# Optimization experiments

Measured on AMD Instinct MI355X. Metric: run time of the kernel, lower is better.

## Reference

```python
import jax, jax.numpy as jnp
import numpy as np

EPS = 1e-8


def setup_inputs() -> dict:
    key = jax.random.key(0)
    k1, k2 = jax.random.split(key)
    N, D, K = 200000, 256, 64
    embeds = jax.random.normal(k1, (N, D), dtype=jnp.float32)
    init = jax.random.uniform(k2, (K, D), dtype=jnp.float32)  # torch.rand(K, n_h)
    beta = jnp.ones((1,), dtype=jnp.float32)
    return {"embeds": embeds, "init": init, "beta": beta, "num_iter": 11}


def reference(embeds, init, beta, num_iter):
    # embeds: [N, D], init: [K, D], beta: scalar temperature
    data_abs = jnp.linalg.norm(embeds, axis=1, keepdims=True)            # [N, 1]
    data_norm = embeds / jnp.maximum(data_abs, EPS)                      # [N, D]
    b = beta.reshape(())
    mu = init
    r = None
    for _ in range(num_iter):  # small fixed iteration count (default 11)
        mu_abs = jnp.linalg.norm(mu, axis=1, keepdims=True)              # [K, 1]
        mu_norm = mu / jnp.maximum(mu_abs, EPS)                          # [K, D]
        dist = data_norm @ mu_norm.T                                     # [N, K]
        r = jax.nn.softmax(b * dist, axis=1)                             # [N, K]
        cluster_r = r.sum(axis=0)                                        # [K]
        cluster_mean = r.T @ embeds                                      # [K, D]
        mu = cluster_mean / cluster_r[:, None]                           # diag(1/cluster_r) @ cluster_mean
    return mu, r
```

## Files before the change

kernel.cpp:

```cpp
#include <hip/hip_runtime.h>
#include <math.h>


#define N_ROWS 200000
#define DIM 256
#define KC 64
#define NUM_ITER 11
#define TR 64
#define NTILES (N_ROWS / TR)
#define EPSV 1e-8f
#define NB 256

typedef _Float16 half8 __attribute__((ext_vector_type(8)));
typedef _Float16 half4 __attribute__((ext_vector_type(4)));
typedef float f32x4 __attribute__((ext_vector_type(4)));

typedef __attribute__((address_space(3))) void as3_void;
typedef __attribute__((address_space(1))) void as1_void;

__device__ __forceinline__ void glds16(const void* g, void* l) {
  __builtin_amdgcn_global_load_lds((const as1_void*)g, (as3_void*)l, 16, 0, 0);
}

__device__ __forceinline__ float wave_reduce_sum(float v) {
#pragma unroll
  for (int off = 32; off > 0; off >>= 1) v += __shfl_xor(v, off, 64);
  return v;
}

__device__ __forceinline__ void barrier_lgkm_only() {
  __builtin_amdgcn_sched_barrier(0);
  asm volatile("s_waitcnt lgkmcnt(0)" ::: "memory");
  __builtin_amdgcn_s_barrier();
  __builtin_amdgcn_sched_barrier(0);
}

__global__ void rn_convert_kernel(const float* __restrict__ embeds,
                                  float* __restrict__ inv_norm,
                                  _Float16* __restrict__ Xh,
                                  const float* __restrict__ init,
                                  float* __restrict__ mu_raw,
                                  float* __restrict__ mu_ssq) {
  if (blockIdx.x == 0) {
    const int c = threadIdx.x >> 2, qq = threadIdx.x & 3;
    const float4* src = (const float4*)(init + (size_t)c * DIM + 64 * qq);
    float4* dst = (float4*)(mu_raw + (size_t)c * DIM + 64 * qq);
    float ss = 0.f;
#pragma unroll
    for (int i = 0; i < 16; ++i) {
      float4 v = src[i];
      dst[i] = v;
      ss = fmaf(v.x, v.x, ss); ss = fmaf(v.y, v.y, ss);
      ss = fmaf(v.z, v.z, ss); ss = fmaf(v.w, v.w, ss);
    }
    mu_ssq[c * 4 + qq] = ss;
  }
  int gw = (blockIdx.x * blockDim.x + threadIdx.x) >> 6;
  int lane = threadIdx.x & 63;
  int nw = (gridDim.x * blockDim.x) >> 6;
  for (int row = gw; row < N_ROWS; row += nw) {
    float4 v = *(const float4*)(embeds + (size_t)row * DIM + 4 * lane);
    float s = v.x * v.x;
    s = fmaf(v.y, v.y, s); s = fmaf(v.z, v.z, s); s = fmaf(v.w, v.w, s);
    s = wave_reduce_sum(s);
    if (lane == 0) inv_norm[row] = 1.0f / fmaxf(sqrtf(s), EPSV);
    half4 h;
    h[0] = (_Float16)v.x; h[1] = (_Float16)v.y; h[2] = (_Float16)v.z; h[3] = (_Float16)v.w;
    *(half4*)(Xh + (size_t)row * DIM + 4 * lane) = h;
  }
}

__device__ __forceinline__ void stage_row512_8(const _Float16* g, _Float16* l,
                                               int wid, int lane) {
#pragma unroll
  for (int ii = 0; ii < 4; ++ii) {
    int i = wid * 4 + ii;
    int row = i * 2 + (lane >> 5);
    int slot = (lane & 31) ^ (row & 7);
    glds16((const char*)g + row * 512 + slot * 16, (char*)l + i * 1024);
  }
}

template <int LAST>
__global__ __launch_bounds__(512, 2) void cluster_main8(
    const _Float16* __restrict__ Xh, const float* __restrict__ inv_norm,
    const float* __restrict__ beta, const float* __restrict__ mu_raw,
    const float* __restrict__ mu_ssq, float* __restrict__ part_cm,
    float* __restrict__ part_crt, float* __restrict__ r_out) {
  __shared__ alignas(16) _Float16 mu_lds[KC * DIM];
  __shared__ alignas(16) _Float16 x_lds[2][TR * DIM];
  __shared__ alignas(16) _Float16 xt_lds[DIM * TR];
  __shared__ alignas(16) _Float16 r_lds[KC * TR];
  __shared__ alignas(16) f32x4 dist_lds[16 * 64];
  __shared__ float cr_lds[4 * KC];

  const int tid = threadIdx.x, wid = tid >> 6, lane = tid & 63;
  const int l15 = lane & 15, h = lane >> 4;
  const int kh = wid >> 2, rg = wid & 3;
  const float b = beta[0];
  const int myrow = 16 * rg + l15;
  const int rb0 = blockIdx.x;

  stage_row512_8(Xh + (size_t)rb0 * TR * DIM, x_lds[0], wid, lane);

  if (tid < KC) {
    const float4 s4 = *(const float4*)&mu_ssq[4 * tid];
    cr_lds[tid] = 1.0f / fmaxf(sqrtf(s4.x + s4.y + s4.z + s4.w), EPSV);
  }
  __syncthreads();
  {
    const float4* mu_raw4 = (const float4*)mu_raw;
#pragma unroll
    for (int i = 0; i < 8; ++i) {
      const int idx = tid + 512 * i;
      const int cl = idx >> 6;
      const int dim0 = (idx & 63) * 4;
      float4 v = mu_raw4[idx];
      const float iv = cr_lds[cl];
      const int sw = dim0 ^ ((cl & 7) << 3);
      half4 hh;
      hh[0] = (_Float16)(v.x * iv); hh[1] = (_Float16)(v.y * iv);
      hh[2] = (_Float16)(v.z * iv); hh[3] = (_Float16)(v.w * iv);
      *(half4*)&mu_lds[cl * DIM + sw] = hh;
    }
  }
  __syncthreads();

  half8 amreg[4][4];
#pragma unroll
  for (int t = 0; t < 4; ++t) {
    const int kb = 128 * kh + 32 * t + 8 * h;
#pragma unroll
    for (int m = 0; m < 4; ++m) {
      const int cl = 16 * m + l15;
      amreg[t][m] = *(const half8*)&mu_lds[cl * DIM + (kb ^ ((cl & 7) << 3))];
    }
  }

  f32x4 acc2[4][2] = {};
  float cr_acc[16] = {};
  int p = 0;
  for (int rb = rb0; rb < NTILES; rb += NB, p ^= 1) {
    const int row0 = rb * TR;
    const int rbn = rb + NB;
    if (rbn < NTILES)
      stage_row512_8(Xh + (size_t)rbn * TR * DIM, x_lds[p ^ 1], wid, lane);

    f32x4 acc1[4] = {};
    const _Float16* xb = x_lds[p];
#pragma unroll
    for (int t = 0; t < 4; ++t) {
      const int kb = 128 * kh + 32 * t + 8 * h;
      half8 bx = *(const half8*)&xb[myrow * DIM + (kb ^ ((myrow & 7) << 3))];
#pragma unroll
      for (int m = 0; m < 4; ++m)
        acc1[m] = __builtin_amdgcn_mfma_f32_16x16x32_f16(amreg[t][m], bx, acc1[m], 0, 0, 0);
    }
    if (kh) {
#pragma unroll
      for (int m = 0; m < 4; ++m) dist_lds[(rg * 4 + m) * 64 + lane] = acc1[m];
    }
    barrier_lgkm_only();

    if (!kh) {
#pragma unroll
      for (int m = 0; m < 4; ++m) acc1[m] += dist_lds[(rg * 4 + m) * 64 + lane];
      const int xr = row0 + myrow;
      const float sc = b * inv_norm[xr];
#pragma unroll
      for (int m = 0; m < 4; ++m)
#pragma unroll
        for (int j = 0; j < 4; ++j) acc1[m][j] *= sc;
      float mx = -1e30f;
#pragma unroll
      for (int m = 0; m < 4; ++m)
#pragma unroll
        for (int j = 0; j < 4; ++j) mx = fmaxf(mx, acc1[m][j]);
      mx = fmaxf(mx, __shfl_xor(mx, 16));
      mx = fmaxf(mx, __shfl_xor(mx, 32));
      float esum = 0.f;
#pragma unroll
      for (int m = 0; m < 4; ++m)
#pragma unroll
        for (int j = 0; j < 4; ++j) {
          float e = __expf(acc1[m][j] - mx);
          acc1[m][j] = e;
          esum += e;
        }
      esum += __shfl_xor(esum, 16);
      esum += __shfl_xor(esum, 32);
      const float rcp = 1.0f / esum;
#pragma unroll
      for (int m = 0; m < 4; ++m) {
#pragma unroll
        for (int j = 0; j < 4; ++j) {
          const float rv = acc1[m][j] * rcp;
          acc1[m][j] = rv;
          const int cl = 16 * m + 4 * h + j;
          cr_acc[m * 4 + j] += rv;
          r_lds[cl * TR + (myrow ^ ((cl & 7) << 3))] = (_Float16)rv;
        }
        if (LAST)
          *(float4*)&r_out[(size_t)xr * KC + 16 * m + 4 * h] = *(float4*)&acc1[m];
      }
    } else {
      const int t8 = tid & 255;
      const int db = t8 >> 3, rb8 = t8 & 7;
      union U { uint4 v; unsigned u[4]; };
      U tin[8];
#pragma unroll
      for (int k2 = 0; k2 < 8; ++k2)
        tin[k2].v = *(const uint4*)&xb[(8 * rb8 + k2) * DIM + ((8 * db) ^ (k2 << 3))];
#pragma unroll
      for (int j = 0; j < 8; ++j) {
        const unsigned sel = (j & 1) ? 0x07060302u : 0x05040100u;
        U o;
#pragma unroll
        for (int m2 = 0; m2 < 4; ++m2)
          o.u[m2] = __builtin_amdgcn_perm(tin[2 * m2 + 1].u[j >> 1],
                                          tin[2 * m2].u[j >> 1], sel);
        *(uint4*)&xt_lds[(8 * db + j) * TR + 8 * (rb8 ^ j)] = o.v;
      }
    }

    barrier_lgkm_only();

#pragma unroll
    for (int t = 0; t < 2; ++t) {
      const int kb = 32 * t + 8 * h;
      half8 ar[4], bx2[2];
#pragma unroll
      for (int m = 0; m < 4; ++m) {
        const int cl = 16 * m + l15;
        ar[m] = *(const half8*)&r_lds[cl * TR + (kb ^ ((cl & 7) << 3))];
      }
#pragma unroll
      for (int n = 0; n < 2; ++n) {
        const int dm = 32 * wid + 16 * n + l15;
        bx2[n] = *(const half8*)&xt_lds[dm * TR + (kb ^ ((dm & 7) << 3))];
      }
#pragma unroll
      for (int m = 0; m < 4; ++m)
#pragma unroll
        for (int n = 0; n < 2; ++n)
          acc2[m][n] = __builtin_amdgcn_mfma_f32_16x16x32_f16(ar[m], bx2[n], acc2[m][n], 0, 0, 0);
    }
    __syncthreads();
  }

  float* pc = part_cm + (size_t)blockIdx.x * (KC * DIM);
#pragma unroll
  for (int m = 0; m < 4; ++m)
#pragma unroll
    for (int n = 0; n < 2; ++n)
#pragma unroll
      for (int j = 0; j < 4; ++j)
        pc[(16 * m + 4 * h + j) * DIM + 32 * wid + 16 * n + l15] = acc2[m][n][j];
  if (wid < 4) {
#pragma unroll
    for (int m = 0; m < 4; ++m)
#pragma unroll
      for (int j = 0; j < 4; ++j) {
        float v = cr_acc[m * 4 + j];
        v += __shfl_xor(v, 1); v += __shfl_xor(v, 2);
        v += __shfl_xor(v, 4); v += __shfl_xor(v, 8);
        if (l15 == 0) cr_lds[wid * KC + 16 * m + 4 * h + j] = v;
      }
  }
  __syncthreads();
  if (wid == 0)
    part_crt[(size_t)lane * NB + blockIdx.x] =
        cr_lds[lane] + cr_lds[KC + lane] + cr_lds[2 * KC + lane] + cr_lds[3 * KC + lane];
}

template <int FINAL>
__global__ void reduce_mu(const float* __restrict__ part_cm,
                          const float* __restrict__ part_crt,
                          float* __restrict__ mu_raw, float* __restrict__ mu_ssq,
                          float* __restrict__ mu_out) {
  const int cl = blockIdx.x, q = blockIdx.y;
  const int tid = threadIdx.x, wid = tid >> 6, lane = tid & 63;
  __shared__ float red2[4 * 64];
  __shared__ float cr4[4];
  float c = part_crt[(size_t)cl * NB + tid];
  c = wave_reduce_sum(c);
  if (lane == 0) cr4[wid] = c;
  float s = 0.f;
  const float* basep =
      part_cm + (size_t)(64 * wid) * (KC * DIM) + cl * DIM + 64 * q + lane;
#pragma unroll 8
  for (int i = 0; i < 64; ++i) s += basep[(size_t)i * (KC * DIM)];
  red2[wid * 64 + lane] = s;
  __syncthreads();
  if (wid == 0) {
    const float crv = cr4[0] + cr4[1] + cr4[2] + cr4[3];
    const float st = red2[lane] + red2[64 + lane] + red2[128 + lane] + red2[192 + lane];
    const float mu = st / crv;
    const int dim = 64 * q + lane;
    if (FINAL) {
      mu_out[cl * DIM + dim] = mu;
    } else {
      mu_raw[cl * DIM + dim] = mu;
      float ss = wave_reduce_sum(mu * mu);
      if (lane == 0) mu_ssq[cl * 4 + q] = ss;
    }
  }
}

__global__ void rownorm_v1(const float* __restrict__ embeds, float* __restrict__ inv_norm) {
  int gw = (blockIdx.x * blockDim.x + threadIdx.x) >> 6;
  int lane = threadIdx.x & 63;
  int nw = (gridDim.x * blockDim.x) >> 6;
  for (int row = gw; row < N_ROWS; row += nw) {
    const float* rp = embeds + (size_t)row * DIM;
    float s = 0.f;
#pragma unroll
    for (int j = 0; j < 4; ++j) { float v = rp[lane + 64 * j]; s = fmaf(v, v, s); }
    s = wave_reduce_sum(s);
    if (lane == 0) inv_norm[row] = 1.0f / fmaxf(sqrtf(s), EPSV);
  }
}
__global__ void prep0_v1(const float* __restrict__ init, float* __restrict__ muT) {
  int k = blockIdx.x, lane = threadIdx.x;
  const float* rp = init + k * DIM;
  float v[4]; float s = 0.f;
#pragma unroll
  for (int j = 0; j < 4; ++j) { v[j] = rp[lane + 64 * j]; s = fmaf(v[j], v[j], s); }
  s = wave_reduce_sum(s);
  float inv = 1.0f / fmaxf(sqrtf(s), EPSV);
#pragma unroll
  for (int j = 0; j < 4; ++j) muT[(lane + 64 * j) * KC + k] = v[j] * inv;
}
__device__ __forceinline__ float wave_reduce_max_v1(float v) {
#pragma unroll
  for (int off = 32; off > 0; off >>= 1) v = fmaxf(v, __shfl_xor(v, off, 64));
  return v;
}
template <int LAST>
__global__ __launch_bounds__(256, 1) void main_v1(
    const float* __restrict__ embeds, const float* __restrict__ inv_norm,
    const float* __restrict__ muT, const float* __restrict__ beta,
    float* __restrict__ part_cm, float* __restrict__ part_cr,
    float* __restrict__ r_out, int nb) {
  __shared__ float mu_l[DIM * KC];
  __shared__ float x_l[TR * DIM];
  __shared__ float r_l[TR * KC];
  __shared__ float cr_l[4 * KC];
  const int tid = threadIdx.x, wid = tid >> 6, lane = tid & 63;
  const float b = beta[0];
  {
    const float4* m4 = (const float4*)muT; float4* ml4 = (float4*)mu_l;
#pragma unroll
    for (int i = 0; i < 16; ++i) ml4[tid + i * 256] = m4[tid + i * 256];
  }
  float acc[64];
#pragma unroll
  for (int i = 0; i < 64; ++i) acc[i] = 0.f;
  float cr = 0.f;
  for (int rb = blockIdx.x; rb < NTILES; rb += nb) {
    const int row0 = rb * TR;
    __syncthreads();
    {
      const float4* x4 = (const float4*)(embeds + (size_t)row0 * DIM);
      float4* xl4 = (float4*)x_l;
#pragma unroll
      for (int i = 0; i < 16; ++i) xl4[tid + i * 256] = x4[tid + i * 256];
    }
    __syncthreads();
    float dist[16];
#pragma unroll
    for (int r = 0; r < 16; ++r) dist[r] = 0.f;
    const int rbase = wid * 16;
    for (int d = 0; d < DIM; d += 4) {
      float mv0 = mu_l[(d + 0) * KC + lane], mv1 = mu_l[(d + 1) * KC + lane];
      float mv2 = mu_l[(d + 2) * KC + lane], mv3 = mu_l[(d + 3) * KC + lane];
#pragma unroll
      for (int r = 0; r < 16; ++r) {
        float4 xv = *(const float4*)&x_l[(rbase + r) * DIM + d];
        dist[r] = fmaf(xv.x, mv0, dist[r]); dist[r] = fmaf(xv.y, mv1, dist[r]);
        dist[r] = fmaf(xv.z, mv2, dist[r]); dist[r] = fmaf(xv.w, mv3, dist[r]);
      }
    }
#pragma unroll
    for (int r = 0; r < 16; ++r) {
      const int row = rbase + r;
      float s = b * (dist[r] * inv_norm[row0 + row]);
      float m = wave_reduce_max_v1(s);
      float e = __expf(s - m);
      float sum = wave_reduce_sum(e);
      float rv = e * (1.0f / sum);
      cr += rv;
      r_l[row * KC + lane] = rv;
      if (LAST) r_out[(size_t)(row0 + row) * KC + lane] = rv;
    }
    __syncthreads();
    const int dbase = wid * 64;
    for (int row = 0; row < TR; ++row) {
      float rv = r_l[row * KC + lane];
#pragma unroll
      for (int dd = 0; dd < 64; dd += 4) {
        float4 xv = *(const float4*)&x_l[row * DIM + dbase + dd];
        acc[dd + 0] = fmaf(rv, xv.x, acc[dd + 0]); acc[dd + 1] = fmaf(rv, xv.y, acc[dd + 1]);
        acc[dd + 2] = fmaf(rv, xv.z, acc[dd + 2]); acc[dd + 3] = fmaf(rv, xv.w, acc[dd + 3]);
      }
    }
  }
  {
    float* pp = part_cm + ((size_t)blockIdx.x * KC + lane) * DIM + wid * 64;
#pragma unroll
    for (int dd = 0; dd < 64; dd += 4)
      *(float4*)&pp[dd] = make_float4(acc[dd], acc[dd + 1], acc[dd + 2], acc[dd + 3]);
    cr_l[wid * KC + lane] = cr;
  }
  __syncthreads();
  if (wid == 0) {
    float c = cr_l[lane] + cr_l[64 + lane] + cr_l[128 + lane] + cr_l[192 + lane];
    part_cr[(size_t)blockIdx.x * KC + lane] = c;
  }
}
template <int FINAL>
__global__ void reduce_v1(const float* __restrict__ part_cm, const float* __restrict__ part_cr,
                          float* __restrict__ muT, float* __restrict__ mu_out, int nb) {
  const int k = blockIdx.x, t = threadIdx.x;
  __shared__ float red[256];
  float s = 0.f;
  for (int bl = 0; bl < nb; ++bl) s += part_cm[((size_t)bl * KC + k) * DIM + t];
  float c = 0.f;
  for (int bl = t; bl < nb; bl += 256) c += part_cr[(size_t)bl * KC + k];
  red[t] = c; __syncthreads();
#pragma unroll
  for (int off = 128; off > 0; off >>= 1) { if (t < off) red[t] += red[t + off]; __syncthreads(); }
  const float crv = red[0]; __syncthreads();
  const float mu = s / crv;
  if (FINAL) { mu_out[k * DIM + t] = mu; return; }
  red[t] = mu * mu; __syncthreads();
#pragma unroll
  for (int off = 128; off > 0; off >>= 1) { if (t < off) red[t] += red[t + off]; __syncthreads(); }
  const float inv = 1.0f / fmaxf(sqrtf(red[0]), EPSV);
  muT[t * KC + k] = mu * inv;
}

extern "C" void kernel_launch(void* const* d_in, const int* in_sizes, int n_in,
                              void* d_out, int out_size, void* d_ws, size_t ws_size,
                              hipStream_t stream) {
  const float* embeds = (const float*)d_in[0];
  const float* init = (const float*)d_in[1];
  const float* beta = (const float*)d_in[2];
  float* out_mu = (float*)d_out;
  float* out_r = out_mu + KC * DIM;
  char* ws = (char*)d_ws;

  const size_t szX = (size_t)N_ROWS * DIM * 2;
  const size_t szInv = (size_t)N_ROWS * 4;
  const size_t szMuR = (size_t)KC * DIM * 4;
  const size_t szSsq = (size_t)KC * 4 * 4;
  const size_t szPC = (size_t)NB * KC * DIM * 4;
  const size_t szPR = (size_t)KC * NB * 4;
  const size_t need = szX + szInv + szMuR + szSsq + szPC + szPR;

  if (ws_size >= need) {
    char* pp = ws;
    _Float16* Xh = (_Float16*)pp; pp += szX;
    float* invn = (float*)pp; pp += szInv;
    float* mu_raw = (float*)pp; pp += szMuR;
    float* mu_ssq = (float*)pp; pp += szSsq;
    float* pcm = (float*)pp; pp += szPC;
    float* pcrt = (float*)pp;

    rn_convert_kernel<<<2048, 256, 0, stream>>>(embeds, invn, Xh, init, mu_raw, mu_ssq);
    for (int it = 0; it < NUM_ITER; ++it) {
      if (it > 0)
        reduce_mu<0><<<dim3(KC, 4), 256, 0, stream>>>(pcm, pcrt, mu_raw, mu_ssq, nullptr);
      if (it == NUM_ITER - 1)
        cluster_main8<1><<<NB, 512, 0, stream>>>(Xh, invn, beta, mu_raw, mu_ssq,
                                                 pcm, pcrt, out_r);
      else
        cluster_main8<0><<<NB, 512, 0, stream>>>(Xh, invn, beta, mu_raw, mu_ssq,
                                                 pcm, pcrt, out_r);
    }
    reduce_mu<1><<<dim3(KC, 4), 256, 0, stream>>>(pcm, pcrt, nullptr, nullptr, out_mu);
  } else {
    float* wsf = (float*)d_ws;
    float* muT = wsf;
    float* invn = muT + DIM * KC;
    size_t avail = ws_size / sizeof(float);
    size_t fixed = (size_t)DIM * KC + N_ROWS;
    size_t per_blk = (size_t)KC * DIM + KC;
    int nb = 256;
    if (avail > fixed) {
      size_t mx = (avail - fixed) / per_blk;
      if (mx < 256) nb = (int)mx;
    } else nb = 1;
    if (nb < 1) nb = 1;
    float* pcm = invn + N_ROWS;
    float* pcr = pcm + (size_t)nb * KC * DIM;

    rownorm_v1<<<2048, 256, 0, stream>>>(embeds, invn);
    prep0_v1<<<KC, 64, 0, stream>>>(init, muT);
    for (int it = 0; it < NUM_ITER; ++it) {
      if (it > 0) reduce_v1<0><<<KC, 256, 0, stream>>>(pcm, pcr, muT, nullptr, nb);
      if (it == NUM_ITER - 1)
        main_v1<1><<<nb, 256, 0, stream>>>(embeds, invn, muT, beta, pcm, pcr, out_r, nb);
      else
        main_v1<0><<<nb, 256, 0, stream>>>(embeds, invn, muT, beta, pcm, pcr, nullptr, nb);
    }
    reduce_v1<1><<<KC, 256, 0, stream>>>(pcm, pcr, muT, out_mu, nb);
  }
}
```

Measured before the change: 498.4 us.

## Restructure cluster kernel to 256-thread blocks with full-K per wave, 512 blocks

```diff
diff --git a/kernel.cpp b/kernel.cpp
--- a/kernel.cpp
+++ b/kernel.cpp
@@ -9,7 +9,7 @@
 #define TR 64
 #define NTILES (N_ROWS / TR)
 #define EPSV 1e-8f
-#define NB 256
+#define NB2 512
 
 typedef _Float16 half8 __attribute__((ext_vector_type(8)));
 typedef _Float16 half4 __attribute__((ext_vector_type(4)));
@@ -70,11 +70,11 @@
   }
 }
 
-__device__ __forceinline__ void stage_row512_8(const _Float16* g, _Float16* l,
+__device__ __forceinline__ void stage_row512_4(const _Float16* g, _Float16* l,
                                                int wid, int lane) {
 #pragma unroll
-  for (int ii = 0; ii < 4; ++ii) {
-    int i = wid * 4 + ii;
+  for (int ii = 0; ii < 8; ++ii) {
+    int i = wid * 8 + ii;
     int row = i * 2 + (lane >> 5);
     int slot = (lane & 31) ^ (row & 7);
     glds16((const char*)g + row * 512 + slot * 16, (char*)l + i * 1024);
@@ -82,26 +82,23 @@
 }
 
 template <int LAST>
-__global__ __launch_bounds__(512, 2) void cluster_main8(
+__global__ __launch_bounds__(256, 2) void cluster_main2b(
     const _Float16* __restrict__ Xh, const float* __restrict__ inv_norm,
     const float* __restrict__ beta, const float* __restrict__ mu_raw,
     const float* __restrict__ mu_ssq, float* __restrict__ part_cm,
     float* __restrict__ part_crt, float* __restrict__ r_out) {
-  __shared__ alignas(16) _Float16 mu_lds[KC * DIM];
-  __shared__ alignas(16) _Float16 x_lds[2][TR * DIM];
+  __shared__ alignas(16) _Float16 x_lds[TR * DIM];
   __shared__ alignas(16) _Float16 xt_lds[DIM * TR];
   __shared__ alignas(16) _Float16 r_lds[KC * TR];
-  __shared__ alignas(16) f32x4 dist_lds[16 * 64];
   __shared__ float cr_lds[4 * KC];
 
   const int tid = threadIdx.x, wid = tid >> 6, lane = tid & 63;
   const int l15 = lane & 15, h = lane >> 4;
-  const int kh = wid >> 2, rg = wid & 3;
   const float b = beta[0];
-  const int myrow = 16 * rg + l15;
+  const int myrow = 16 * wid + l15;
   const int rb0 = blockIdx.x;
 
-  stage_row512_8(Xh + (size_t)rb0 * TR * DIM, x_lds[0], wid, lane);
+  stage_row512_4(Xh + (size_t)rb0 * TR * DIM, x_lds, wid, lane);
 
   if (tid < KC) {
     const float4 s4 = *(const float4*)&mu_ssq[4 * tid];
@@ -111,8 +108,8 @@
   {
     const float4* mu_raw4 = (const float4*)mu_raw;
 #pragma unroll
-    for (int i = 0; i < 8; ++i) {
-      const int idx = tid + 512 * i;
+    for (int i = 0; i < 16; ++i) {
+      const int idx = tid + 256 * i;
       const int cl = idx >> 6;
       const int dim0 = (idx & 63) * 4;
       float4 v = mu_raw4[idx];
@@ -121,52 +118,40 @@
       half4 hh;
       hh[0] = (_Float16)(v.x * iv); hh[1] = (_Float16)(v.y * iv);
       hh[2] = (_Float16)(v.z * iv); hh[3] = (_Float16)(v.w * iv);
-      *(half4*)&mu_lds[cl * DIM + sw] = hh;
+      *(half4*)&xt_lds[cl * DIM + sw] = hh;
     }
   }
   __syncthreads();
-
-  half8 amreg[4][4];
-#pragma unroll
-  for (int t = 0; t < 4; ++t) {
-    const int kb = 128 * kh + 32 * t + 8 * h;
+  half8 amreg[8][4];
+#pragma unroll
+  for (int t = 0; t < 8; ++t) {
+    const int kb = 32 * t + 8 * h;
 #pragma unroll
     for (int m = 0; m < 4; ++m) {
       const int cl = 16 * m + l15;
-      amreg[t][m] = *(const half8*)&mu_lds[cl * DIM + (kb ^ ((cl & 7) << 3))];
-    }
-  }
-
-  f32x4 acc2[4][2] = {};
+      amreg[t][m] = *(const half8*)&xt_lds[cl * DIM + (kb ^ ((cl & 7) << 3))];
+    }
+  }
+  barrier_lgkm_only();
+
+  f32x4 acc2[4][4] = {};
   float cr_acc[16] = {};
-  int p = 0;
-  for (int rb = rb0; rb < NTILES; rb += NB, p ^= 1) {
-    const int row0 = rb * TR;
-    const int rbn = rb + NB;
-    if (rbn < NTILES)
-      stage_row512_8(Xh + (size_t)rbn * TR * DIM, x_lds[p ^ 1], wid, lane);
+  for (int rb = rb0; rb < NTILES; rb += NB2) {
+    const int xr = rb * TR + myrow;
+    const float invn = inv_norm[xr];
 
     f32x4 acc1[4] = {};
-    const _Float16* xb = x_lds[p];
-#pragma unroll
-    for (int t = 0; t < 4; ++t) {
-      const int kb = 128 * kh + 32 * t + 8 * h;
-      half8 bx = *(const half8*)&xb[myrow * DIM + (kb ^ ((myrow & 7) << 3))];
+#pragma unroll
+    for (int t = 0; t < 8; ++t) {
+      const int kb = 32 * t + 8 * h;
+      half8 bx = *(const half8*)&x_lds[myrow * DIM + (kb ^ ((myrow & 7) << 3))];
 #pragma unroll
       for (int m = 0; m < 4; ++m)
         acc1[m] = __builtin_amdgcn_mfma_f32_16x16x32_f16(amreg[t][m], bx, acc1[m], 0, 0, 0);
     }
-    if (kh) {
-#pragma unroll
-      for (int m = 0; m < 4; ++m) dist_lds[(rg * 4 + m) * 64 + lane] = acc1[m];
-    }
-    barrier_lgkm_only();
-
-    if (!kh) {
-#pragma unroll
-      for (int m = 0; m < 4; ++m) acc1[m] += dist_lds[(rg * 4 + m) * 64 + lane];
-      const int xr = row0 + myrow;
-      const float sc = b * inv_norm[xr];
+
+    {
+      const float sc = b * invn;
 #pragma unroll
       for (int m = 0; m < 4; ++m)
 #pragma unroll
@@ -203,14 +188,15 @@
         if (LAST)
           *(float4*)&r_out[(size_t)xr * KC + 16 * m + 4 * h] = *(float4*)&acc1[m];
       }
-    } else {
-      const int t8 = tid & 255;
-      const int db = t8 >> 3, rb8 = t8 & 7;
+    }
+
+    {
+      const int db = tid >> 3, rb8 = tid & 7;
       union U { uint4 v; unsigned u[4]; };
       U tin[8];
 #pragma unroll
       for (int k2 = 0; k2 < 8; ++k2)
-        tin[k2].v = *(const uint4*)&xb[(8 * rb8 + k2) * DIM + ((8 * db) ^ (k2 << 3))];
+        tin[k2].v = *(const uint4*)&x_lds[(8 * rb8 + k2) * DIM + ((8 * db) ^ (k2 << 3))];
 #pragma unroll
       for (int j = 0; j < 8; ++j) {
         const unsigned sel = (j & 1) ? 0x07060302u : 0x05040100u;
@@ -225,24 +211,27 @@
 
     barrier_lgkm_only();
 
+    if (rb + NB2 < NTILES)
+      stage_row512_4(Xh + (size_t)(rb + NB2) * TR * DIM, x_lds, wid, lane);
+
 #pragma unroll
     for (int t = 0; t < 2; ++t) {
       const int kb = 32 * t + 8 * h;
-      half8 ar[4], bx2[2];
+      half8 ar[4], bx2[4];
 #pragma unroll
       for (int m = 0; m < 4; ++m) {
         const int cl = 16 * m + l15;
         ar[m] = *(const half8*)&r_lds[cl * TR + (kb ^ ((cl & 7) << 3))];
       }
 #pragma unroll
-      for (int n = 0; n < 2; ++n) {
-        const int dm = 32 * wid + 16 * n + l15;
+      for (int n = 0; n < 4; ++n) {
+        const int dm = 64 * wid + 16 * n + l15;
         bx2[n] = *(const half8*)&xt_lds[dm * TR + (kb ^ ((dm & 7) << 3))];
       }
 #pragma unroll
       for (int m = 0; m < 4; ++m)
 #pragma unroll
-        for (int n = 0; n < 2; ++n)
+        for (int n = 0; n < 4; ++n)
           acc2[m][n] = __builtin_amdgcn_mfma_f32_16x16x32_f16(ar[m], bx2[n], acc2[m][n], 0, 0, 0);
     }
     __syncthreads();
@@ -252,24 +241,22 @@
 #pragma unroll
   for (int m = 0; m < 4; ++m)
 #pragma unroll
-    for (int n = 0; n < 2; ++n)
+    for (int n = 0; n < 4; ++n)
 #pragma unroll
       for (int j = 0; j < 4; ++j)
-        pc[(16 * m + 4 * h + j) * DIM + 32 * wid + 16 * n + l15] = acc2[m][n][j];
-  if (wid < 4) {
-#pragma unroll
-    for (int m = 0; m < 4; ++m)
-#pragma unroll
-      for (int j = 0; j < 4; ++j) {
-        float v = cr_acc[m * 4 + j];
-        v += __shfl_xor(v, 1); v += __shfl_xor(v, 2);
-        v += __shfl_xor(v, 4); v += __shfl_xor(v, 8);
-        if (l15 == 0) cr_lds[wid * KC + 16 * m + 4 * h + j] = v;
-      }
-  }
+        pc[(16 * m + 4 * h + j) * DIM + 64 * wid + 16 * n + l15] = acc2[m][n][j];
+#pragma unroll
+  for (int m = 0; m < 4; ++m)
+#pragma unroll
+    for (int j = 0; j < 4; ++j) {
+      float v = cr_acc[m * 4 + j];
+      v += __shfl_xor(v, 1); v += __shfl_xor(v, 2);
+      v += __shfl_xor(v, 4); v += __shfl_xor(v, 8);
+      if (l15 == 0) cr_lds[wid * KC + 16 * m + 4 * h + j] = v;
+    }
   __syncthreads();
   if (wid == 0)
-    part_crt[(size_t)lane * NB + blockIdx.x] =
+    part_crt[(size_t)lane * NB2 + blockIdx.x] =
         cr_lds[lane] + cr_lds[KC + lane] + cr_lds[2 * KC + lane] + cr_lds[3 * KC + lane];
 }
 
@@ -282,14 +269,15 @@
   const int tid = threadIdx.x, wid = tid >> 6, lane = tid & 63;
   __shared__ float red2[4 * 64];
   __shared__ float cr4[4];
-  float c = part_crt[(size_t)cl * NB + tid];
+  float c = part_crt[(size_t)cl * NB2 + tid] +
+            part_crt[(size_t)cl * NB2 + 256 + tid];
   c = wave_reduce_sum(c);
   if (lane == 0) cr4[wid] = c;
   float s = 0.f;
   const float* basep =
-      part_cm + (size_t)(64 * wid) * (KC * DIM) + cl * DIM + 64 * q + lane;
+      part_cm + (size_t)(128 * wid) * (KC * DIM) + cl * DIM + 64 * q + lane;
 #pragma unroll 8
-  for (int i = 0; i < 64; ++i) s += basep[(size_t)i * (KC * DIM)];
+  for (int i = 0; i < 128; ++i) s += basep[(size_t)i * (KC * DIM)];
   red2[wid * 64 + lane] = s;
   __syncthreads();
   if (wid == 0) {
@@ -307,6 +295,7 @@
   }
 }
 
+#define NTILES64 NTILES
 __global__ void rownorm_v1(const float* __restrict__ embeds, float* __restrict__ inv_norm) {
   int gw = (blockIdx.x * blockDim.x + threadIdx.x) >> 6;
   int lane = threadIdx.x & 63;
@@ -357,7 +346,7 @@
 #pragma unroll
   for (int i = 0; i < 64; ++i) acc[i] = 0.f;
   float cr = 0.f;
-  for (int rb = blockIdx.x; rb < NTILES; rb += nb) {
+  for (int rb = blockIdx.x; rb < NTILES64; rb += nb) {
     const int row0 = rb * TR;
     __syncthreads();
     {
@@ -454,8 +443,8 @@
   const size_t szInv = (size_t)N_ROWS * 4;
   const size_t szMuR = (size_t)KC * DIM * 4;
   const size_t szSsq = (size_t)KC * 4 * 4;
-  const size_t szPC = (size_t)NB * KC * DIM * 4;
-  const size_t szPR = (size_t)KC * NB * 4;
+  const size_t szPC = (size_t)NB2 * KC * DIM * 4;
+  const size_t szPR = (size_t)KC * NB2 * 4;
   const size_t need = szX + szInv + szMuR + szSsq + szPC + szPR;
 
   if (ws_size >= need) {
@@ -472,11 +461,11 @@
       if (it > 0)
         reduce_mu<0><<<dim3(KC, 4), 256, 0, stream>>>(pcm, pcrt, mu_raw, mu_ssq, nullptr);
       if (it == NUM_ITER - 1)
-        cluster_main8<1><<<NB, 512, 0, stream>>>(Xh, invn, beta, mu_raw, mu_ssq,
-                                                 pcm, pcrt, out_r);
+        cluster_main2b<1><<<NB2, 256, 0, stream>>>(Xh, invn, beta, mu_raw, mu_ssq,
+                                                   pcm, pcrt, out_r);
       else
-        cluster_main8<0><<<NB, 512, 0, stream>>>(Xh, invn, beta, mu_raw, mu_ssq,
-                                                 pcm, pcrt, out_r);
+        cluster_main2b<0><<<NB2, 256, 0, stream>>>(Xh, invn, beta, mu_raw, mu_ssq,
+                                                   pcm, pcrt, out_r);
     }
     reduce_mu<1><<<dim3(KC, 4), 256, 0, stream>>>(pcm, pcrt, nullptr, nullptr, out_mu);
   } else {
```

Measured after the change: 1.038 ms. 2.08x slower.

## Fuse fp16 conversion and row-norm pass into the first clustering iteration

Applied to the files above, without the earlier changes.

```diff
diff --git a/kernel.cpp b/kernel.cpp
--- a/kernel.cpp
+++ b/kernel.cpp
@@ -35,41 +35,6 @@
   __builtin_amdgcn_sched_barrier(0);
 }
 
-__global__ void rn_convert_kernel(const float* __restrict__ embeds,
-                                  float* __restrict__ inv_norm,
-                                  _Float16* __restrict__ Xh,
-                                  const float* __restrict__ init,
-                                  float* __restrict__ mu_raw,
-                                  float* __restrict__ mu_ssq) {
-  if (blockIdx.x == 0) {
-    const int c = threadIdx.x >> 2, qq = threadIdx.x & 3;
-    const float4* src = (const float4*)(init + (size_t)c * DIM + 64 * qq);
-    float4* dst = (float4*)(mu_raw + (size_t)c * DIM + 64 * qq);
-    float ss = 0.f;
-#pragma unroll
-    for (int i = 0; i < 16; ++i) {
-      float4 v = src[i];
-      dst[i] = v;
-      ss = fmaf(v.x, v.x, ss); ss = fmaf(v.y, v.y, ss);
-      ss = fmaf(v.z, v.z, ss); ss = fmaf(v.w, v.w, ss);
-    }
-    mu_ssq[c * 4 + qq] = ss;
-  }
-  int gw = (blockIdx.x * blockDim.x + threadIdx.x) >> 6;
-  int lane = threadIdx.x & 63;
-  int nw = (gridDim.x * blockDim.x) >> 6;
-  for (int row = gw; row < N_ROWS; row += nw) {
-    float4 v = *(const float4*)(embeds + (size_t)row * DIM + 4 * lane);
-    float s = v.x * v.x;
-    s = fmaf(v.y, v.y, s); s = fmaf(v.z, v.z, s); s = fmaf(v.w, v.w, s);
-    s = wave_reduce_sum(s);
-    if (lane == 0) inv_norm[row] = 1.0f / fmaxf(sqrtf(s), EPSV);
-    half4 h;
-    h[0] = (_Float16)v.x; h[1] = (_Float16)v.y; h[2] = (_Float16)v.z; h[3] = (_Float16)v.w;
-    *(half4*)(Xh + (size_t)row * DIM + 4 * lane) = h;
-  }
-}
-
 __device__ __forceinline__ void stage_row512_8(const _Float16* g, _Float16* l,
                                                int wid, int lane) {
 #pragma unroll
@@ -79,6 +44,236 @@
     int slot = (lane & 31) ^ (row & 7);
     glds16((const char*)g + row * 512 + slot * 16, (char*)l + i * 1024);
   }
+}
+
+__global__ __launch_bounds__(512, 1) void cluster_first(
+    const float* __restrict__ embeds, const float* __restrict__ init,
+    const float* __restrict__ beta, _Float16* __restrict__ Xh,
+    float* __restrict__ inv_norm, float* __restrict__ part_cm,
+    float* __restrict__ part_crt) {
+  __shared__ alignas(16) _Float16 x_lds[2][TR * DIM];
+  __shared__ alignas(16) _Float16 xt_lds[DIM * TR];
+  __shared__ alignas(16) _Float16 mu_lds[KC * DIM];
+  __shared__ alignas(16) _Float16 r_lds[KC * TR];
+  __shared__ alignas(16) f32x4 dist_lds[16 * 64];
+  __shared__ float cr_lds[4 * KC];
+  __shared__ float inv_lds[TR];
+
+  float* x32 = (float*)&x_lds[0][0];
+  _Float16* xtile = xt_lds;
+  _Float16* xtr = &x_lds[0][0];
+
+  const int tid = threadIdx.x, wid = tid >> 6, lane = tid & 63;
+  const int l15 = lane & 15, h = lane >> 4;
+  const int kh = wid >> 2, rg = wid & 3;
+  const float b = beta[0];
+  const int myrow = 16 * rg + l15;
+  const int rb0 = blockIdx.x;
+
+  {
+    const int cl = tid >> 3, sub = tid & 7;
+    float ss = 0.f;
+#pragma unroll
+    for (int j = 0; j < 8; ++j) {
+      float4 v = *(const float4*)(init + (size_t)cl * DIM + sub * 32 + 4 * j);
+      ss = fmaf(v.x, v.x, ss); ss = fmaf(v.y, v.y, ss);
+      ss = fmaf(v.z, v.z, ss); ss = fmaf(v.w, v.w, ss);
+    }
+    ss += __shfl_xor(ss, 1); ss += __shfl_xor(ss, 2); ss += __shfl_xor(ss, 4);
+    if (sub == 0) cr_lds[cl] = ss;
+  }
+  __syncthreads();
+  if (tid < KC) cr_lds[tid] = 1.0f / fmaxf(sqrtf(cr_lds[tid]), EPSV);
+  __syncthreads();
+  {
+    const float4* init4 = (const float4*)init;
+#pragma unroll
+    for (int i = 0; i < 8; ++i) {
+      const int idx = tid + 512 * i;
+      const int cl = idx >> 6;
+      const int dim0 = (idx & 63) * 4;
+      float4 v = init4[idx];
+      const float iv = cr_lds[cl];
+      const int sw = dim0 ^ ((cl & 7) << 3);
+      half4 hh;
+      hh[0] = (_Float16)(v.x * iv); hh[1] = (_Float16)(v.y * iv);
+      hh[2] = (_Float16)(v.z * iv); hh[3] = (_Float16)(v.w * iv);
+      *(half4*)&mu_lds[cl * DIM + sw] = hh;
+    }
+  }
+  __syncthreads();
+  half8 amreg[4][4];
+#pragma unroll
+  for (int t = 0; t < 4; ++t) {
+    const int kb = 128 * kh + 32 * t + 8 * h;
+#pragma unroll
+    for (int m = 0; m < 4; ++m) {
+      const int cl = 16 * m + l15;
+      amreg[t][m] = *(const half8*)&mu_lds[cl * DIM + (kb ^ ((cl & 7) << 3))];
+    }
+  }
+
+  f32x4 acc2[4][2] = {};
+  float cr_acc[16] = {};
+  for (int rb = rb0; rb < NTILES; rb += NB) {
+#pragma unroll
+    for (int ii = 0; ii < 8; ++ii) {
+      const int row = wid * 8 + ii;
+      const int slot = lane ^ (row & 7);
+      glds16((const char*)embeds + (size_t)(rb * TR + row) * 1024 + slot * 16,
+             (char*)x32 + row * 1024);
+    }
+    __syncthreads();
+
+    {
+      const int row = tid >> 3, sub = tid & 7;
+      float ss = 0.f;
+      half8 hh[4];
+#pragma unroll
+      for (int i2 = 0; i2 < 8; ++i2) {
+        const int g = sub * 8 + i2;
+        float4 v = *(const float4*)((const char*)x32 + row * 1024 +
+                                    ((g ^ (row & 7)) * 16));
+        ss = fmaf(v.x, v.x, ss); ss = fmaf(v.y, v.y, ss);
+        ss = fmaf(v.z, v.z, ss); ss = fmaf(v.w, v.w, ss);
+        _Float16* hp = (_Float16*)&hh[i2 >> 1] + (i2 & 1) * 4;
+        hp[0] = (_Float16)v.x; hp[1] = (_Float16)v.y;
+        hp[2] = (_Float16)v.z; hp[3] = (_Float16)v.w;
+      }
+#pragma unroll
+      for (int j = 0; j < 4; ++j) {
+        const int slot = (sub * 4 + j) ^ (row & 7);
+        *(half8*)((char*)xtile + row * 512 + slot * 16) = hh[j];
+        *(float4*)((char*)Xh + (size_t)(rb * TR + row) * 512 + sub * 64 + j * 16) =
+            *(float4*)&hh[j];
+      }
+      ss += __shfl_xor(ss, 1); ss += __shfl_xor(ss, 2); ss += __shfl_xor(ss, 4);
+      if (sub == 0) {
+        const float iv = 1.0f / fmaxf(sqrtf(ss), EPSV);
+        inv_lds[row] = iv;
+        inv_norm[rb * TR + row] = iv;
+      }
+    }
+    barrier_lgkm_only();
+
+    f32x4 acc1[4] = {};
+#pragma unroll
+    for (int t = 0; t < 4; ++t) {
+      const int kb = 128 * kh + 32 * t + 8 * h;
+      half8 bx = *(const half8*)&xtile[myrow * DIM + (kb ^ ((myrow & 7) << 3))];
+#pragma unroll
+      for (int m = 0; m < 4; ++m)
+        acc1[m] = __builtin_amdgcn_mfma_f32_16x16x32_f16(amreg[t][m], bx, acc1[m], 0, 0, 0);
+    }
+    if (kh) {
+#pragma unroll
+      for (int m = 0; m < 4; ++m) dist_lds[(rg * 4 + m) * 64 + lane] = acc1[m];
+    }
+    barrier_lgkm_only();
+
+    if (!kh) {
+#pragma unroll
+      for (int m = 0; m < 4; ++m) acc1[m] += dist_lds[(rg * 4 + m) * 64 + lane];
+      const float sc = b * inv_lds[myrow];
+#pragma unroll
+      for (int m = 0; m < 4; ++m)
+#pragma unroll
+        for (int j = 0; j < 4; ++j) acc1[m][j] *= sc;
+      float mx = -1e30f;
+#pragma unroll
+      for (int m = 0; m < 4; ++m)
+#pragma unroll
+        for (int j = 0; j < 4; ++j) mx = fmaxf(mx, acc1[m][j]);
+      mx = fmaxf(mx, __shfl_xor(mx, 16));
+      mx = fmaxf(mx, __shfl_xor(mx, 32));
+      float esum = 0.f;
+#pragma unroll
+      for (int m = 0; m < 4; ++m)
+#pragma unroll
+        for (int j = 0; j < 4; ++j) {
+          float e = __expf(acc1[m][j] - mx);
+          acc1[m][j] = e;
+          esum += e;
+        }
+      esum += __shfl_xor(esum, 16);
+      esum += __shfl_xor(esum, 32);
+      const float rcp = 1.0f / esum;
+#pragma unroll
+      for (int m = 0; m < 4; ++m)
+#pragma unroll
+        for (int j = 0; j < 4; ++j) {
+          const float rv = acc1[m][j] * rcp;
+          const int cl = 16 * m + 4 * h + j;
+          cr_acc[m * 4 + j] += rv;
+          r_lds[cl * TR + (myrow ^ ((cl & 7) << 3))] = (_Float16)rv;
+        }
+    } else {
+      const int t8 = tid & 255;
+      const int db = t8 >> 3, rb8 = t8 & 7;
+      union U { uint4 v; unsigned u[4]; };
+      U tin[8];
+#pragma unroll
+      for (int k2 = 0; k2 < 8; ++k2)
+        tin[k2].v = *(const uint4*)&xtile[(8 * rb8 + k2) * DIM + ((8 * db) ^ (k2 << 3))];
+#pragma unroll
+      for (int j = 0; j < 8; ++j) {
+        const unsigned sel = (j & 1) ? 0x07060302u : 0x05040100u;
+        U o;
+#pragma unroll
+        for (int m2 = 0; m2 < 4; ++m2)
+          o.u[m2] = __builtin_amdgcn_perm(tin[2 * m2 + 1].u[j >> 1],
+                                          tin[2 * m2].u[j >> 1], sel);
+        *(uint4*)&xtr[(8 * db + j) * TR + 8 * (rb8 ^ j)] = o.v;
+      }
+    }
+    barrier_lgkm_only();
+
+#pragma unroll
+    for (int t = 0; t < 2; ++t) {
+      const int kb = 32 * t + 8 * h;
+      half8 ar[4], bx2[2];
+#pragma unroll
+      for (int m = 0; m < 4; ++m) {
+        const int cl = 16 * m + l15;
+        ar[m] = *(const half8*)&r_lds[cl * TR + (kb ^ ((cl & 7) << 3))];
+      }
+#pragma unroll
+      for (int n = 0; n < 2; ++n) {
+        const int dm = 32 * wid + 16 * n + l15;
+        bx2[n] = *(const half8*)&xtr[dm * TR + (kb ^ ((dm & 7) << 3))];
+      }
+#pragma unroll
+      for (int m = 0; m < 4; ++m)
+#pragma unroll
+        for (int n = 0; n < 2; ++n)
+          acc2[m][n] = __builtin_amdgcn_mfma_f32_16x16x32_f16(ar[m], bx2[n], acc2[m][n], 0, 0, 0);
+    }
+    __syncthreads();
+  }
+
+  float* pc = part_cm + (size_t)blockIdx.x * (KC * DIM);
+#pragma unroll
+  for (int m = 0; m < 4; ++m)
+#pragma unroll
+    for (int n = 0; n < 2; ++n)
+#pragma unroll
+      for (int j = 0; j < 4; ++j)
+        pc[(16 * m + 4 * h + j) * DIM + 32 * wid + 16 * n + l15] = acc2[m][n][j];
+  if (wid < 4) {
+#pragma unroll
+    for (int m = 0; m < 4; ++m)
+#pragma unroll
+      for (int j = 0; j < 4; ++j) {
+        float v = cr_acc[m * 4 + j];
+        v += __shfl_xor(v, 1); v += __shfl_xor(v, 2);
+        v += __shfl_xor(v, 4); v += __shfl_xor(v, 8);
+        if (l15 == 0) cr_lds[wid * KC + 16 * m + 4 * h + j] = v;
+      }
+  }
+  __syncthreads();
+  if (wid == 0)
+    part_crt[(size_t)lane * NB + blockIdx.x] =
+        cr_lds[lane] + cr_lds[KC + lane] + cr_lds[2 * KC + lane] + cr_lds[3 * KC + lane];
 }
 
 template <int LAST>
@@ -467,10 +662,9 @@
     float* pcm = (float*)pp; pp += szPC;
     float* pcrt = (float*)pp;
 
-    rn_convert_kernel<<<2048, 256, 0, stream>>>(embeds, invn, Xh, init, mu_raw, mu_ssq);
-    for (int it = 0; it < NUM_ITER; ++it) {
-      if (it > 0)
-        reduce_mu<0><<<dim3(KC, 4), 256, 0, stream>>>(pcm, pcrt, mu_raw, mu_ssq, nullptr);
+    cluster_first<<<NB, 512, 0, stream>>>(embeds, init, beta, Xh, invn, pcm, pcrt);
+    for (int it = 1; it < NUM_ITER; ++it) {
+      reduce_mu<0><<<dim3(KC, 4), 256, 0, stream>>>(pcm, pcrt, mu_raw, mu_ssq, nullptr);
       if (it == NUM_ITER - 1)
         cluster_main8<1><<<NB, 512, 0, stream>>>(Xh, invn, beta, mu_raw, mu_ssq,
                                                  pcm, pcrt, out_r);
```

Measured after the change: 490.7 us, median of 2. Within noise of the previous version (-1.5%).
